# Optimization experiments

Measured on AMD Instinct MI355X. Metric: run time of the kernel, lower is better.

Reference implementation:

```python
import jax, jax.numpy as jnp
import numpy as np

B, S, D, H = 4, 2048, 1024, 16
HD = D // H

def setup_inputs() -> dict:
    key = jax.random.key(0)
    ks = jax.random.split(key, 10)
    s = 1.0 / np.sqrt(D)
    inp = {
        'x': jax.random.normal(ks[0], (B, S, D), dtype=jnp.float32),
        'attention_mask': jnp.ones((B, S), dtype=jnp.int32),
        'Wq': jax.random.uniform(ks[1], (D, D), jnp.float32, -s, s),
        'bq': jax.random.uniform(ks[2], (D,), jnp.float32, -s, s),
        'Wk': jax.random.uniform(ks[3], (D, D), jnp.float32, -s, s),
        'bk': jax.random.uniform(ks[4], (D,), jnp.float32, -s, s),
        'Wv': jax.random.uniform(ks[5], (D, D), jnp.float32, -s, s),
        'bv': jax.random.uniform(ks[6], (D,), jnp.float32, -s, s),
        'Wo': jax.random.uniform(ks[7], (D, D), jnp.float32, -s, s),
        'bo': jax.random.uniform(ks[8], (D,), jnp.float32, -s, s),
    }
    return inp

def reference(x, Wq, bq, Wk, bk, Wv, bv, Wo, bo, attention_mask):
    scale = HD ** -0.5
    # torch Linear: y = x @ W^T + b
    def proj(W, b):
        return (x @ W.T + b).reshape(B, S, H, HD).transpose(0, 2, 1, 3)  # [B,H,S,hd]
    q = proj(Wq, bq)
    k = proj(Wk, bk)
    v = proj(Wv, bv)
    scores = jnp.einsum('bhqd,bhkd->bhqk', q, k) * scale  # [B,H,S,S]
    causal = jnp.triu(jnp.ones((S, S), dtype=bool), k=1)
    scores = jnp.where(causal, -jnp.inf, scores)
    pad = (attention_mask == 0)[:, None, None, :]  # [B,1,1,S]
    scores = jnp.where(pad, jnp.float32(-1e9), scores)
    probs = jax.nn.softmax(scores, axis=-1)
    out = jnp.einsum('bhqk,bhkd->bhqd', probs, v)  # [B,H,S,hd]
    out = out.transpose(0, 2, 1, 3).reshape(B, S, D)
    return out @ Wo.T + bo
```

## Files before the change

kernel.cpp:

```cpp
#include <hip/hip_runtime.h>
#include <hip/hip_bf16.h>

typedef unsigned short u16;
typedef float f32x4 __attribute__((ext_vector_type(4)));
typedef __bf16 bf16x8 __attribute__((ext_vector_type(8)));

#define BB 4
#define SS 2048
#define DD 1024
#define HH 16
#define HDD 64
#define MM (BB*SS)

__device__ __forceinline__ u16 f2bf(float f){
    union { float f; unsigned int i; } v; v.f = f;
    unsigned int i = v.i;
    return (u16)((i + 0x7FFFu + ((i >> 16) & 1u)) >> 16);
}
__device__ __forceinline__ ushort2 pk2(float a, float b){
    union { __hip_bfloat162 h; ushort2 u; } v;
    float2 t; t.x = a; t.y = b;
    v.h = __float22bfloat162_rn(t);
    return v.u;
}
__device__ __forceinline__ ushort4 pk4(float a, float b, float c, float d){
    ushort2 lo = pk2(a, b), hi = pk2(c, d);
    ushort4 r; r.x = lo.x; r.y = lo.y; r.z = hi.x; r.w = hi.y;
    return r;
}
__device__ __forceinline__ void gl2lds16(const void* g, void* l){
    __builtin_amdgcn_global_load_lds(
        (const __attribute__((address_space(1))) void*)g,
        (__attribute__((address_space(3))) void*)l, 16, 0, 0);
}

__device__ __forceinline__ void cvt8(const float* __restrict__ src,
                                     u16* __restrict__ dst, size_t i)
{
    const float4 a = *(const float4*)&src[i];
    const float4 b = *(const float4*)&src[i + 4];
    ushort4 lo = pk4(a.x, a.y, a.z, a.w);
    ushort4 hi = pk4(b.x, b.y, b.z, b.w);
    uint4 o;
    o.x = (unsigned)lo.x | ((unsigned)lo.y << 16);
    o.y = (unsigned)lo.z | ((unsigned)lo.w << 16);
    o.z = (unsigned)hi.x | ((unsigned)hi.y << 16);
    o.w = (unsigned)hi.z | ((unsigned)hi.w << 16);
    *(uint4*)&dst[i] = o;
}

__global__ __launch_bounds__(256) void cvt_k(const float* __restrict__ src,
                                             u16* __restrict__ dst)
{
    const size_t i = ((size_t)blockIdx.x * 256 + threadIdx.x) * 8;
    cvt8(src, dst, i);
}

__global__ __launch_bounds__(256) void cvtw_k(
    const float* __restrict__ W0, const float* __restrict__ W1,
    const float* __restrict__ W2, const float* __restrict__ W3,
    u16* __restrict__ dst)
{
    const float* src = blockIdx.y == 0 ? W0 : (blockIdx.y == 1 ? W1 :
                        (blockIdx.y == 2 ? W2 : W3));
    u16* d = dst + (size_t)blockIdx.y * (size_t)DD * DD;
    const size_t i = ((size_t)blockIdx.x * 256 + threadIdx.x) * 8;
    cvt8(src, d, i);
}

template<bool WB>
__device__ __forceinline__ void gemm_core_t(const u16* __restrict__ A,
                                            const float* __restrict__ Wf,
                                            const u16* __restrict__ Wb,
                                            f32x4 (&acc)[4][4],
                                            u16* At, u16* Bt,
                                            int m0, int n0, int tid)
{
    const int lane = tid & 63, w = tid >> 6;
    const int quad = lane >> 4, l15 = lane & 15;
    const int wm = w >> 1, wn = w & 1;
    const int arow = lane >> 2;
    const int acol = (lane & 3) * 8;

    for (int k0 = 0; k0 < DD; k0 += 32) {
        __syncthreads();
        #pragma unroll
        for (int c = 0; c < 2; ++c) {
            const int ch = w * 2 + c;
            gl2lds16(&A[(size_t)(m0 + ch * 16 + arow) * DD + k0 + acol], &At[ch * 512]);
        }
        if (WB) {
            #pragma unroll
            for (int c = 0; c < 2; ++c) {
                const int ch = w * 2 + c;
                gl2lds16(&Wb[(size_t)(n0 + ch * 16 + arow) * DD + k0 + acol], &Bt[ch * 512]);
            }
        } else {
            #pragma unroll
            for (int it = 0; it < 2; ++it) {
                const int c = tid + it * 256;
                const int row = c >> 2, cc = (c & 3) * 8;
                const size_t woff = (size_t)(n0 + row) * DD + k0 + cc;
                const float4 u0 = *(const float4*)&Wf[woff];
                const float4 u1 = *(const float4*)&Wf[woff + 4];
                ushort4 lo = pk4(u0.x, u0.y, u0.z, u0.w);
                ushort4 hi = pk4(u1.x, u1.y, u1.z, u1.w);
                uint4 o;
                o.x = (unsigned)lo.x | ((unsigned)lo.y << 16);
                o.y = (unsigned)lo.z | ((unsigned)lo.w << 16);
                o.z = (unsigned)hi.x | ((unsigned)hi.y << 16);
                o.w = (unsigned)hi.z | ((unsigned)hi.w << 16);
                *(uint4*)&Bt[row * 32 + cc] = o;
            }
        }
        __syncthreads();
        bf16x8 af[4], bfr[4];
        #pragma unroll
        for (int i = 0; i < 4; ++i)
            af[i] = *(const bf16x8*)&At[(wm * 64 + i * 16 + l15) * 32 + quad * 8];
        #pragma unroll
        for (int j = 0; j < 4; ++j)
            bfr[j] = *(const bf16x8*)&Bt[(wn * 64 + j * 16 + l15) * 32 + quad * 8];
        #pragma unroll
        for (int i = 0; i < 4; ++i)
            #pragma unroll
            for (int j = 0; j < 4; ++j)
                acc[i][j] = __builtin_amdgcn_mfma_f32_16x16x32_bf16(af[i], bfr[j], acc[i][j], 0, 0, 0);
    }
}

template<bool WB>
__global__ __launch_bounds__(256, 4) void gemm_qkv_k(
    const u16* __restrict__ x,
    const float* __restrict__ Wq, const float* __restrict__ bq,
    const float* __restrict__ Wk, const float* __restrict__ bk,
    const float* __restrict__ Wv, const float* __restrict__ bv,
    const u16* __restrict__ Wqb, const u16* __restrict__ Wkb,
    const u16* __restrict__ Wvb,
    u16* __restrict__ Q, u16* __restrict__ K, u16* __restrict__ V)
{
    __shared__ alignas(16) u16 At[128 * 32];
    __shared__ alignas(16) u16 Bt[128 * 32];
    const int tid = threadIdx.x, lane = tid & 63, w = tid >> 6;
    const int quad = lane >> 4, l15 = lane & 15;
    const int wm = w >> 1, wn = w & 1;
    const int z = blockIdx.z;
    const float* Wm = z == 0 ? Wq : (z == 1 ? Wk : Wv);
    const u16* Wmb = z == 0 ? Wqb : (z == 1 ? Wkb : Wvb);
    const float* bias = z == 0 ? bq : (z == 1 ? bk : bv);
    u16* Out = z == 0 ? Q : (z == 1 ? K : V);
    const int m0 = blockIdx.x * 128, n0 = blockIdx.y * 128;

    f32x4 acc[4][4];
    #pragma unroll
    for (int i = 0; i < 4; ++i)
        #pragma unroll
        for (int j = 0; j < 4; ++j) acc[i][j] = (f32x4)(0.0f);

    gemm_core_t<WB>(x, Wm, Wmb, acc, At, Bt, m0, n0, tid);

    float bs[4];
    #pragma unroll
    for (int j = 0; j < 4; ++j) bs[j] = bias[n0 + wn * 64 + j * 16 + l15];

    const int b = m0 / SS;
    const int h = (n0 + wn * 64) / HDD;
    const size_t base = ((size_t)(b * HH + h)) * SS * HDD;
    #pragma unroll
    for (int i = 0; i < 4; ++i) {
        #pragma unroll
        for (int r = 0; r < 4; ++r) {
            const int s = (m0 % SS) + wm * 64 + i * 16 + quad * 4 + r;
            #pragma unroll
            for (int j = 0; j < 4; ++j) {
                const int hd = j * 16 + l15;
                Out[base + (size_t)s * HDD + hd] = f2bf(acc[i][j][r] + bs[j]);
            }
        }
    }
}

template<bool WB>
__global__ __launch_bounds__(256, 4) void gemm_out_k(
    const u16* __restrict__ A, const float* __restrict__ Wo,
    const float* __restrict__ bo, const u16* __restrict__ Wob,
    float* __restrict__ Out)
{
    __shared__ alignas(16) u16 At[128 * 32];
    __shared__ alignas(16) u16 Bt[128 * 32];
    const int tid = threadIdx.x, lane = tid & 63, w = tid >> 6;
    const int quad = lane >> 4, l15 = lane & 15;
    const int wm = w >> 1, wn = w & 1;
    const int m0 = blockIdx.x * 128, n0 = blockIdx.y * 128;

    f32x4 acc[4][4];
    #pragma unroll
    for (int i = 0; i < 4; ++i)
        #pragma unroll
        for (int j = 0; j < 4; ++j) acc[i][j] = (f32x4)(0.0f);

    gemm_core_t<WB>(A, Wo, Wob, acc, At, Bt, m0, n0, tid);

    float bs[4];
    #pragma unroll
    for (int j = 0; j < 4; ++j) bs[j] = bo[n0 + wn * 64 + j * 16 + l15];

    #pragma unroll
    for (int i = 0; i < 4; ++i) {
        #pragma unroll
        for (int r = 0; r < 4; ++r) {
            const int m = m0 + wm * 64 + i * 16 + quad * 4 + r;
            #pragma unroll
            for (int j = 0; j < 4; ++j) {
                const int n = n0 + wn * 64 + j * 16 + l15;
                Out[(size_t)m * DD + n] = acc[i][j][r] + bs[j];
            }
        }
    }
}

#define QT 256
#define KT 64
#define LDPV 66

#define LOG2E 1.4426950408889634f

__device__ __forceinline__ int swz128(int row, int bcol){
    return row * 128 + (bcol ^ ((row & 7) << 4));
}

__global__ __launch_bounds__(512, 3) void attn_k(
    const u16* __restrict__ Q, const u16* __restrict__ K,
    const u16* __restrict__ V, const int* __restrict__ mask,
    u16* __restrict__ AO)
{
    __shared__ alignas(16) u16 QPs[QT * 64];
    __shared__ alignas(16) u16 Ks[KT * 64];
    __shared__ alignas(16) u16 Vs[HDD * LDPV];
    __shared__ float padf[KT];

    const int tid = threadIdx.x, lane = tid & 63, w = tid >> 6;
    const int quad = lane >> 4, l15 = lane & 15;
    const int bh = blockIdx.x;
    const int y = blockIdx.y;
    const int qt = (y < 4) ? (7 - y) : (y - 4);
    const int b = bh >> 4, h = bh & 15;
    const int q0 = qt * QT;
    const size_t hoff = (size_t)bh * SS * HDD;
    const u16* Qh = Q + hoff;
    const u16* Kh = K + hoff;
    const u16* Vh = V + hoff;
    const int nkt = (q0 + QT) / KT;
    const float scale2 = 0.125f * LOG2E;

    for (int c = tid; c < QT * 8; c += 512) {
        const int row = c >> 3, cc = c & 7;
        *(uint4*)((char*)QPs + swz128(row, cc * 16)) =
            *(const uint4*)&Qh[(size_t)(q0 + row) * HDD + cc * 8];
    }
    __syncthreads();

    bf16x8 bQ[2][2];
    #pragma unroll
    for (int j = 0; j < 2; ++j)
        #pragma unroll
        for (int ks = 0; ks < 2; ++ks)
            bQ[j][ks] = *(const bf16x8*)((const char*)QPs +
                swz128(w * 32 + j * 16 + l15, ks * 64 + quad * 16));

    float m_run[2] = { -1e30f, -1e30f };
    float l_run[2] = { 0.f, 0.f };
    f32x4 o[4][2];
    #pragma unroll
    for (int i = 0; i < 4; ++i)
        #pragma unroll
        for (int j = 0; j < 2; ++j) o[i][j] = (f32x4)(0.0f);

    for (int kt = 0; kt < nkt; ++kt) {
        const int kt0 = kt * KT;
        __syncthreads();

        if (tid < 256) {
            #pragma unroll
            for (int it = 0; it < 2; ++it) {
                const int c = tid + it * 256;
                const int row = c >> 3, cc = c & 7;
                *(uint4*)((char*)Ks + swz128(row, cc * 16)) =
                    *(const uint4*)&Kh[(size_t)(kt0 + row) * HDD + cc * 8];
            }
        } else if (tid < 384) {
            const int t = tid - 256;
            const int kq = t >> 3;
            const int c0 = (t & 7) * 8;
            uint4 r0 = *(const uint4*)&Vh[(size_t)(kt0 + kq * 4 + 0) * HDD + c0];
            uint4 r1 = *(const uint4*)&Vh[(size_t)(kt0 + kq * 4 + 1) * HDD + c0];
            uint4 r2 = *(const uint4*)&Vh[(size_t)(kt0 + kq * 4 + 2) * HDD + c0];
            uint4 r3 = *(const uint4*)&Vh[(size_t)(kt0 + kq * 4 + 3) * HDD + c0];
            const u16* e0 = (const u16*)&r0;
            const u16* e1 = (const u16*)&r1;
            const u16* e2 = (const u16*)&r2;
            const u16* e3 = (const u16*)&r3;
            #pragma unroll
            for (int e = 0; e < 8; ++e) {
                ushort4 pkv; pkv.x = e0[e]; pkv.y = e1[e]; pkv.z = e2[e]; pkv.w = e3[e];
                *(ushort4*)&Vs[(c0 + e) * LDPV + kq * 4] = pkv;
            }
        } else if (tid < 448) {
            const int t = tid - 384;
            padf[t] = (mask[b * SS + kt0 + t] == 0) ? -1e9f : 0.0f;
        }
        __syncthreads();

        f32x4 sc[4][2];
        #pragma unroll
        for (int i = 0; i < 4; ++i)
            #pragma unroll
            for (int j = 0; j < 2; ++j) sc[i][j] = (f32x4)(0.0f);
        __builtin_amdgcn_s_setprio(1);
        #pragma unroll
        for (int ks = 0; ks < 2; ++ks) {
            bf16x8 aK[4];
            #pragma unroll
            for (int i = 0; i < 4; ++i)
                aK[i] = *(const bf16x8*)((const char*)Ks +
                    swz128(i * 16 + l15, ks * 64 + quad * 16));
            #pragma unroll
            for (int i = 0; i < 4; ++i)
                #pragma unroll
                for (int j = 0; j < 2; ++j)
                    sc[i][j] = __builtin_amdgcn_mfma_f32_16x16x32_bf16(aK[i], bQ[j][ks], sc[i][j], 0, 0, 0);
        }
        __builtin_amdgcn_s_setprio(0);

        f32x4 pb[4];
        #pragma unroll
        for (int i = 0; i < 4; ++i)
            pb[i] = *(const f32x4*)&padf[i * 16 + quad * 4];

        #pragma unroll
        for (int j = 0; j < 2; ++j) {
            const int qrow = q0 + w * 32 + j * 16 + l15;
            const bool needC = (kt0 + KT - 1) > (q0 + w * 32 + j * 16);
            float mx = -1e9f;
            if (needC) {
                #pragma unroll
                for (int i = 0; i < 4; ++i)
                    #pragma unroll
                    for (int r = 0; r < 4; ++r) {
                        const int kpg = kt0 + i * 16 + quad * 4 + r;
                        float s = fmaf(sc[i][j][r], scale2, pb[i][r]);
                        s = (kpg > qrow) ? -1e9f : s;
                        sc[i][j][r] = s; mx = fmaxf(mx, s);
                    }
            } else {
                #pragma unroll
                for (int i = 0; i < 4; ++i)
                    #pragma unroll
                    for (int r = 0; r < 4; ++r) {
                        float s = fmaf(sc[i][j][r], scale2, pb[i][r]);
                        sc[i][j][r] = s; mx = fmaxf(mx, s);
                    }
            }
            mx = fmaxf(mx, __shfl_xor(mx, 16, 64));
            mx = fmaxf(mx, __shfl_xor(mx, 32, 64));
            float nm = m_run[j];
            if (!__all(mx <= nm + 8.f)) {
                nm = fmaxf(nm, mx);
                const float alpha = __builtin_exp2f(m_run[j] - nm);
                m_run[j] = nm;
                l_run[j] *= alpha;
                #pragma unroll
                for (int i = 0; i < 4; ++i)
                    #pragma unroll
                    for (int r = 0; r < 4; ++r) o[i][j][r] *= alpha;
            }
            float rs = 0.f;
            #pragma unroll
            for (int i = 0; i < 4; ++i) {
                float p0 = __builtin_exp2f(sc[i][j][0] - nm);
                float p1 = __builtin_exp2f(sc[i][j][1] - nm);
                float p2 = __builtin_exp2f(sc[i][j][2] - nm);
                float p3 = __builtin_exp2f(sc[i][j][3] - nm);
                rs += (p0 + p1) + (p2 + p3);
                *(ushort4*)((char*)QPs + swz128(w * 32 + j * 16 + l15, i * 32 + quad * 8)) =
                    pk4(p0, p1, p2, p3);
            }
            l_run[j] += rs;
        }
        asm volatile("s_waitcnt lgkmcnt(0)" ::: "memory");

        __builtin_amdgcn_s_setprio(1);
        #pragma unroll
        for (int ks = 0; ks < 2; ++ks) {
            bf16x8 aV[4], bP[2];
            #pragma unroll
            for (int i = 0; i < 4; ++i)
                aV[i] = *(const bf16x8*)&Vs[(i * 16 + l15) * LDPV + ks * 32 + quad * 8];
            #pragma unroll
            for (int j = 0; j < 2; ++j)
                bP[j] = *(const bf16x8*)((const char*)QPs +
                    swz128(w * 32 + j * 16 + l15, ks * 64 + quad * 16));
            #pragma unroll
            for (int i = 0; i < 4; ++i)
                #pragma unroll
                for (int j = 0; j < 2; ++j)
                    o[i][j] = __builtin_amdgcn_mfma_f32_16x16x32_bf16(aV[i], bP[j], o[i][j], 0, 0, 0);
        }
        __builtin_amdgcn_s_setprio(0);
    }

    #pragma unroll
    for (int j = 0; j < 2; ++j) {
        float l = l_run[j];
        l += __shfl_xor(l, 16, 64);
        l += __shfl_xor(l, 32, 64);
        const float inv = (l > 0.f) ? (1.f / l) : 0.f;
        const int s = q0 + w * 32 + j * 16 + l15;
        const size_t rb = ((size_t)(b * SS + s)) * DD + h * HDD;
        #pragma unroll
        for (int i = 0; i < 4; ++i)
            *(ushort4*)&AO[rb + i * 16 + quad * 4] =
                pk4(o[i][j][0] * inv, o[i][j][1] * inv, o[i][j][2] * inv, o[i][j][3] * inv);
    }
}

extern "C" void kernel_launch(void* const* d_in, const int* in_sizes, int n_in,
                              void* d_out, int out_size, void* d_ws, size_t ws_size,
                              hipStream_t stream)
{
    const float* x  = (const float*)d_in[0];
    const int* mask = (const int*)d_in[1];
    const float* Wq = (const float*)d_in[2];
    const float* bq = (const float*)d_in[3];
    const float* Wk = (const float*)d_in[4];
    const float* bk = (const float*)d_in[5];
    const float* Wv = (const float*)d_in[6];
    const float* bv = (const float*)d_in[7];
    const float* Wo = (const float*)d_in[8];
    const float* bo = (const float*)d_in[9];
    float* out = (float*)d_out;

    u16* ws = (u16*)d_ws;
    const size_t NE = (size_t)MM * DD;
    const size_t WE = (size_t)DD * DD;
    if (ws_size < 4 * NE * sizeof(u16)) return;
    const bool wb = ws_size >= (4 * NE + 4 * WE) * sizeof(u16);

    u16* Qb = ws;
    u16* Kb = ws + NE;
    u16* Vb = ws + 2 * NE;
    u16* Ab = ws + 3 * NE;

    dim3 blk(256);
    cvt_k<<<dim3(NE / 2048), blk, 0, stream>>>(x, Ab);
    if (wb) {
        u16* Wbase = ws + 4 * NE;
        cvtw_k<<<dim3(WE / 2048, 4), blk, 0, stream>>>(Wq, Wk, Wv, Wo, Wbase);
        gemm_qkv_k<true><<<dim3(MM / 128, DD / 128, 3), blk, 0, stream>>>(
            Ab, Wq, bq, Wk, bk, Wv, bv,
            Wbase, Wbase + WE, Wbase + 2 * WE, Qb, Kb, Vb);
        attn_k<<<dim3(BB * HH, SS / QT), dim3(512), 0, stream>>>(Qb, Kb, Vb, mask, Ab);
        gemm_out_k<true><<<dim3(MM / 128, DD / 128), blk, 0, stream>>>(
            Ab, Wo, bo, Wbase + 3 * WE, out);
    } else {
        gemm_qkv_k<false><<<dim3(MM / 128, DD / 128, 3), blk, 0, stream>>>(
            Ab, Wq, bq, Wk, bk, Wv, bv,
            nullptr, nullptr, nullptr, Qb, Kb, Vb);
        attn_k<<<dim3(BB * HH, SS / QT), dim3(512), 0, stream>>>(Qb, Kb, Vb, mask, Ab);
        gemm_out_k<false><<<dim3(MM / 128, DD / 128), blk, 0, stream>>>(
            Ab, Wo, bo, nullptr, out);
    }
}
```

Before: 317.5 us.

## Stage bf16 weights in output/Q scratch and skip masked warp tiles in attention

```diff
diff --git a/kernel.cpp b/kernel.cpp
--- a/kernel.cpp
+++ b/kernel.cpp
@@ -56,25 +56,28 @@
     cvt8(src, dst, i);
 }
 
-__global__ __launch_bounds__(256) void cvtw_k(
+__global__ __launch_bounds__(256) void cvtw3_k(
     const float* __restrict__ W0, const float* __restrict__ W1,
-    const float* __restrict__ W2, const float* __restrict__ W3,
-    u16* __restrict__ dst)
-{
-    const float* src = blockIdx.y == 0 ? W0 : (blockIdx.y == 1 ? W1 :
-                        (blockIdx.y == 2 ? W2 : W3));
+    const float* __restrict__ W2, u16* __restrict__ dst)
+{
+    const float* src = blockIdx.y == 0 ? W0 : (blockIdx.y == 1 ? W1 : W2);
     u16* d = dst + (size_t)blockIdx.y * (size_t)DD * DD;
     const size_t i = ((size_t)blockIdx.x * 256 + threadIdx.x) * 8;
     cvt8(src, d, i);
 }
 
-template<bool WB>
-__device__ __forceinline__ void gemm_core_t(const u16* __restrict__ A,
-                                            const float* __restrict__ Wf,
-                                            const u16* __restrict__ Wb,
-                                            f32x4 (&acc)[4][4],
-                                            u16* At, u16* Bt,
-                                            int m0, int n0, int tid)
+__global__ __launch_bounds__(256) void cvtw1_k(const float* __restrict__ W,
+                                               u16* __restrict__ dst)
+{
+    const size_t i = ((size_t)blockIdx.x * 256 + threadIdx.x) * 8;
+    cvt8(W, dst, i);
+}
+
+__device__ __forceinline__ void gemm_core(const u16* __restrict__ A,
+                                          const u16* __restrict__ Wb,
+                                          f32x4 (&acc)[4][4],
+                                          u16* At, u16* Bt,
+                                          int m0, int n0, int tid)
 {
     const int lane = tid & 63, w = tid >> 6;
     const int quad = lane >> 4, l15 = lane & 15;
@@ -89,29 +92,10 @@
             const int ch = w * 2 + c;
             gl2lds16(&A[(size_t)(m0 + ch * 16 + arow) * DD + k0 + acol], &At[ch * 512]);
         }
-        if (WB) {
-            #pragma unroll
-            for (int c = 0; c < 2; ++c) {
-                const int ch = w * 2 + c;
-                gl2lds16(&Wb[(size_t)(n0 + ch * 16 + arow) * DD + k0 + acol], &Bt[ch * 512]);
-            }
-        } else {
-            #pragma unroll
-            for (int it = 0; it < 2; ++it) {
-                const int c = tid + it * 256;
-                const int row = c >> 2, cc = (c & 3) * 8;
-                const size_t woff = (size_t)(n0 + row) * DD + k0 + cc;
-                const float4 u0 = *(const float4*)&Wf[woff];
-                const float4 u1 = *(const float4*)&Wf[woff + 4];
-                ushort4 lo = pk4(u0.x, u0.y, u0.z, u0.w);
-                ushort4 hi = pk4(u1.x, u1.y, u1.z, u1.w);
-                uint4 o;
-                o.x = (unsigned)lo.x | ((unsigned)lo.y << 16);
-                o.y = (unsigned)lo.z | ((unsigned)lo.w << 16);
-                o.z = (unsigned)hi.x | ((unsigned)hi.y << 16);
-                o.w = (unsigned)hi.z | ((unsigned)hi.w << 16);
-                *(uint4*)&Bt[row * 32 + cc] = o;
-            }
+        #pragma unroll
+        for (int c = 0; c < 2; ++c) {
+            const int ch = w * 2 + c;
+            gl2lds16(&Wb[(size_t)(n0 + ch * 16 + arow) * DD + k0 + acol], &Bt[ch * 512]);
         }
         __syncthreads();
         bf16x8 af[4], bfr[4];
@@ -129,12 +113,10 @@
     }
 }
 
-template<bool WB>
 __global__ __launch_bounds__(256, 4) void gemm_qkv_k(
     const u16* __restrict__ x,
-    const float* __restrict__ Wq, const float* __restrict__ bq,
-    const float* __restrict__ Wk, const float* __restrict__ bk,
-    const float* __restrict__ Wv, const float* __restrict__ bv,
+    const float* __restrict__ bq, const float* __restrict__ bk,
+    const float* __restrict__ bv,
     const u16* __restrict__ Wqb, const u16* __restrict__ Wkb,
     const u16* __restrict__ Wvb,
     u16* __restrict__ Q, u16* __restrict__ K, u16* __restrict__ V)
@@ -145,7 +127,6 @@
     const int quad = lane >> 4, l15 = lane & 15;
     const int wm = w >> 1, wn = w & 1;
     const int z = blockIdx.z;
-    const float* Wm = z == 0 ? Wq : (z == 1 ? Wk : Wv);
     const u16* Wmb = z == 0 ? Wqb : (z == 1 ? Wkb : Wvb);
     const float* bias = z == 0 ? bq : (z == 1 ? bk : bv);
     u16* Out = z == 0 ? Q : (z == 1 ? K : V);
@@ -157,7 +138,7 @@
         #pragma unroll
         for (int j = 0; j < 4; ++j) acc[i][j] = (f32x4)(0.0f);
 
-    gemm_core_t<WB>(x, Wm, Wmb, acc, At, Bt, m0, n0, tid);
+    gemm_core(x, Wmb, acc, At, Bt, m0, n0, tid);
 
     float bs[4];
     #pragma unroll
@@ -180,11 +161,9 @@
     }
 }
 
-template<bool WB>
 __global__ __launch_bounds__(256, 4) void gemm_out_k(
-    const u16* __restrict__ A, const float* __restrict__ Wo,
-    const float* __restrict__ bo, const u16* __restrict__ Wob,
-    float* __restrict__ Out)
+    const u16* __restrict__ A, const float* __restrict__ bo,
+    const u16* __restrict__ Wob, float* __restrict__ Out)
 {
     __shared__ alignas(16) u16 At[128 * 32];
     __shared__ alignas(16) u16 Bt[128 * 32];
@@ -199,7 +178,7 @@
         #pragma unroll
         for (int j = 0; j < 4; ++j) acc[i][j] = (f32x4)(0.0f);
 
-    gemm_core_t<WB>(A, Wo, Wob, acc, At, Bt, m0, n0, tid);
+    gemm_core(A, Wob, acc, At, Bt, m0, n0, tid);
 
     float bs[4];
     #pragma unroll
@@ -252,6 +231,7 @@
     const u16* Vh = V + hoff;
     const int nkt = (q0 + QT) / KT;
     const float scale2 = 0.125f * LOG2E;
+    const int wrow_end = q0 + w * 32 + 32;
 
     for (int c = tid; c < QT * 8; c += 512) {
         const int row = c >> 3, cc = c & 7;
@@ -311,6 +291,7 @@
         }
         __syncthreads();
 
+        if (kt0 < wrow_end) {
         f32x4 sc[4][2];
         #pragma unroll
         for (int i = 0; i < 4; ++i)
@@ -407,6 +388,7 @@
                     o[i][j] = __builtin_amdgcn_mfma_f32_16x16x32_bf16(aV[i], bP[j], o[i][j], 0, 0, 0);
         }
         __builtin_amdgcn_s_setprio(0);
+        }
     }
 
     #pragma unroll
@@ -444,30 +426,20 @@
     const size_t NE = (size_t)MM * DD;
     const size_t WE = (size_t)DD * DD;
     if (ws_size < 4 * NE * sizeof(u16)) return;
-    const bool wb = ws_size >= (4 * NE + 4 * WE) * sizeof(u16);
 
     u16* Qb = ws;
     u16* Kb = ws + NE;
     u16* Vb = ws + 2 * NE;
     u16* Ab = ws + 3 * NE;
 
+    u16* Wscr = (u16*)d_out;
+
     dim3 blk(256);
     cvt_k<<<dim3(NE / 2048), blk, 0, stream>>>(x, Ab);
-    if (wb) {
-        u16* Wbase = ws + 4 * NE;
-        cvtw_k<<<dim3(WE / 2048, 4), blk, 0, stream>>>(Wq, Wk, Wv, Wo, Wbase);
-        gemm_qkv_k<true><<<dim3(MM / 128, DD / 128, 3), blk, 0, stream>>>(
-            Ab, Wq, bq, Wk, bk, Wv, bv,
-            Wbase, Wbase + WE, Wbase + 2 * WE, Qb, Kb, Vb);
-        attn_k<<<dim3(BB * HH, SS / QT), dim3(512), 0, stream>>>(Qb, Kb, Vb, mask, Ab);
-        gemm_out_k<true><<<dim3(MM / 128, DD / 128), blk, 0, stream>>>(
-            Ab, Wo, bo, Wbase + 3 * WE, out);
-    } else {
-        gemm_qkv_k<false><<<dim3(MM / 128, DD / 128, 3), blk, 0, stream>>>(
-            Ab, Wq, bq, Wk, bk, Wv, bv,
-            nullptr, nullptr, nullptr, Qb, Kb, Vb);
-        attn_k<<<dim3(BB * HH, SS / QT), dim3(512), 0, stream>>>(Qb, Kb, Vb, mask, Ab);
-        gemm_out_k<false><<<dim3(MM / 128, DD / 128), blk, 0, stream>>>(
-            Ab, Wo, bo, nullptr, out);
-    }
-}
+    cvtw3_k<<<dim3(WE / 2048, 3), blk, 0, stream>>>(Wq, Wk, Wv, Wscr);
+    gemm_qkv_k<<<dim3(MM / 128, DD / 128, 3), blk, 0, stream>>>(
+        Ab, bq, bk, bv, Wscr, Wscr + WE, Wscr + 2 * WE, Qb, Kb, Vb);
+    attn_k<<<dim3(BB * HH, SS / QT), dim3(512), 0, stream>>>(Qb, Kb, Vb, mask, Ab);
+    cvtw1_k<<<dim3(WE / 2048), blk, 0, stream>>>(Wo, Qb);
+    gemm_out_k<<<dim3(MM / 128, DD / 128), blk, 0, stream>>>(Ab, bo, Qb, out);
+}
```

Measured after the change: 318.3 us. Within noise of the previous version (+0.3%).
